# Performance work log

Measured on AMD Instinct MI355X. Metric: run time of the kernel, lower is better.

Reference implementation:

```python
import jax, jax.numpy as jnp
import numpy as np

B, N, DIM, H, D = 1, 1024, 512, 8, 64
BC, BS, K, W = 16, 16, 8, 256   # compress blk, selection blk, top-k blocks, sliding window
C = N // BC                     # number of compression / selection blocks
SCALE = D ** -0.5
EPS = 1e-6
NEG = -1e30


def rmsnorm(x):
    return x * jax.lax.rsqrt(jnp.mean(x * x, axis=-1, keepdims=True) + EPS)


def rope(x):  # x: [B,H,N,D], GPT-NeoX style half rotation
    half = D // 2
    inv = 1.0 / (10000.0 ** (jnp.arange(half, dtype=jnp.float32) / half))
    ang = jnp.arange(x.shape[2], dtype=jnp.float32)[:, None] * inv
    cos, sin = jnp.cos(ang), jnp.sin(ang)
    x1, x2 = x[..., :half], x[..., half:]
    return jnp.concatenate([x1 * cos - x2 * sin, x2 * cos + x1 * sin], axis=-1).astype(x.dtype)


def setup_inputs():
    key = jax.random.key(0)
    ks = jax.random.split(key, 24)
    w = lambda k, shape, fan: jax.random.normal(k, shape, jnp.float32) * (fan ** -0.5)
    return {
        'x':  jax.random.normal(ks[0], (B, N, DIM), jnp.float32),
        've': jax.random.normal(ks[1], (B, N, DIM), jnp.float32),
        'x0': jax.random.normal(ks[2], (B, N, DIM), jnp.float32),
        'lambdas': jnp.array([1.0, 0.0], jnp.float32),
        'Wq': w(ks[3], (DIM, H * D), DIM),
        'Wk': w(ks[4], (DIM, H * D), DIM),
        'Wv': w(ks[5], (DIM, H * D), DIM),
        'Wo': w(ks[6], (H * D, DIM), H * D),
        'Wg': w(ks[7], (DIM, 3 * H), DIM),
        'k_pos': w(ks[8], (H, BC, D), D),
        'v_pos': w(ks[9], (H, BC, D), D),
        'Wck': w(ks[10], (BC * D, D), BC * D),
        'bck': jnp.zeros((D,), jnp.float32),
        'Wcv': w(ks[11], (BC * D, D), BC * D),
        'bcv': jnp.zeros((D,), jnp.float32),
        'k_mem': w(ks[12], (H, 1, D), D),
        'v_mem': w(ks[13], (H, 1, D), D),
        'W1': w(ks[14], (DIM, 4 * DIM), DIM),
        'W2': w(ks[15], (4 * DIM, DIM), 4 * DIM),
    }


def _nsa_attn(xn, Wq, Wk, Wv, Wo, Wg, k_pos, v_pos, Wck, bck, Wcv, bcv, k_mem, v_mem):
    q = (xn @ Wq).reshape(B, N, H, D).transpose(0, 2, 1, 3)   # [B,H,N,D]
    k = (xn @ Wk).reshape(B, N, H, D).transpose(0, 2, 1, 3)
    v = (xn @ Wv).reshape(B, N, H, D).transpose(0, 2, 1, 3)
    q, k = rope(q), rope(k)
    i_idx = jnp.arange(N)

    # ---- compressed branch: pool kv into blocks via learned linear + intra-block pos emb ----
    kb = k.reshape(B, H, C, BC, D) + k_pos[None, :, None]
    vb = v.reshape(B, H, C, BC, D) + v_pos[None, :, None]
    ck = kb.reshape(B, H, C, BC * D) @ Wck + bck              # [B,H,C,D]
    cv = vb.reshape(B, H, C, BC * D) @ Wcv + bcv
    ckf = jnp.concatenate([jnp.broadcast_to(k_mem[None], (B, H, 1, D)), ck], axis=2)
    cvf = jnp.concatenate([jnp.broadcast_to(v_mem[None], (B, H, 1, D)), cv], axis=2)
    csim = jnp.einsum('bhid,bhjd->bhij', q, ckf) * SCALE      # [B,H,N,C+1]
    past = ((jnp.arange(C) + 1) * BC - 1)[None, :] < i_idx[:, None]   # block fully in the past
    cmask = jnp.concatenate([jnp.ones((N, 1), bool), past], axis=1)   # mem kv always visible
    cattn = jax.nn.softmax(jnp.where(cmask[None, None], csim, NEG), axis=-1)
    c_out = jnp.einsum('bhij,bhjd->bhid', cattn, cvf)

    # ---- fine selection branch: top-K blocks by compressed attention importance ----
    imp = jnp.where(past[None, None], cattn[..., 1:], NEG)    # [B,H,N,C]
    vals, sel = jax.lax.top_k(imp, K)                         # [B,H,N,K]
    valid = vals >= 0.0                                       # drop picks among masked blocks
    kb_f = k.reshape(B, H, C, BS, D)
    vb_f = v.reshape(B, H, C, BS, D)
    k_sel = jnp.take_along_axis(kb_f[:, :, None], sel[..., None, None], axis=3)  # [B,H,N,K,BS,D]
    v_sel = jnp.take_along_axis(vb_f[:, :, None], sel[..., None, None], axis=3)
    own = i_idx // BS                                         # query's own block, causal inside
    k_fine = jnp.concatenate([k_sel, kb_f[:, :, own][:, :, :, None]], axis=3)    # [B,H,N,K+1,BS,D]
    v_fine = jnp.concatenate([v_sel, vb_f[:, :, own][:, :, :, None]], axis=3)
    offs = jnp.arange(BS)
    m_sel = (sel[..., None] * BS + offs <= i_idx[None, None, :, None, None]) & valid[..., None]
    m_own = jnp.broadcast_to((own[:, None] * BS + offs <= i_idx[:, None])[None, None, :, None], (B, H, N, 1, BS))
    m_fine = jnp.concatenate([m_sel, m_own], axis=3)
    fsim = jnp.where(m_fine, jnp.einsum('bhnd,bhnksd->bhnks', q, k_fine) * SCALE, NEG)
    fattn = jax.nn.softmax(fsim.reshape(B, H, N, (K + 1) * BS), axis=-1).reshape(B, H, N, K + 1, BS)
    f_out = jnp.einsum('bhnks,bhnksd->bhnd', fattn, v_fine)

    # ---- sliding window branch ----
    smask = (i_idx[None, :] <= i_idx[:, None]) & (i_idx[:, None] - i_idx[None, :] < W)
    ssim = jnp.where(smask[None, None], jnp.einsum('bhid,bhjd->bhij', q, k) * SCALE, NEG)
    s_out = jnp.einsum('bhij,bhjd->bhid', jax.nn.softmax(ssim, axis=-1), v)

    # ---- per-head sigmoid gates combine the three strategies ----
    gates = jax.nn.sigmoid(xn @ Wg).reshape(B, N, H, 3).transpose(0, 2, 1, 3)  # [B,H,N,3]
    o = gates[..., 0:1] * c_out + gates[..., 1:2] * f_out + gates[..., 2:3] * s_out
    return o.transpose(0, 2, 1, 3).reshape(B, N, H * D) @ Wo


def reference(x, ve, x0, lambdas, Wq, Wk, Wv, Wo, Wg, k_pos, v_pos, Wck, bck, Wcv, bcv, k_mem, v_mem, W1, W2):
    # ve is accepted by NSABlock.forward but never consumed in this block
    x = lambdas[0] * x + lambdas[1] * x0
    x = x + _nsa_attn(rmsnorm(x), Wq, Wk, Wv, Wo, Wg, k_pos, v_pos, Wck, bck, Wcv, bcv, k_mem, v_mem)
    x = x + jnp.square(jax.nn.relu(rmsnorm(x) @ W1)) @ W2
    return x
```

## Files before the change

kernel.cpp:

```cpp
#include <hip/hip_runtime.h>
#include <math.h>

#define NTOK 1024
#define DIMM 512
#define NH 8
#define HD 64
#define BCB 16
#define BSB 16
#define KSEL 8
#define WWIN 256
#define CBLK 64
#define SCALE 0.125f
#define EPSV 1e-6f
#define NEGV -1e30f

typedef short bf16x8 __attribute__((ext_vector_type(8)));
typedef float f32x4 __attribute__((ext_vector_type(4)));

__device__ inline ushort f2b(float f) {
  union { float f; unsigned int u; } c; c.f = f;
  unsigned int u = c.u;
  return (ushort)((u + 0x7FFFu + ((u >> 16) & 1u)) >> 16);
}
__device__ inline float b2f(ushort h) {
  union { unsigned int u; float f; } c; c.u = ((unsigned int)h) << 16;
  return c.f;
}

__device__ inline float wred_max(float v) {
#pragma unroll
  for (int off = 1; off < 64; off <<= 1) v = fmaxf(v, __shfl_xor(v, off));
  return v;
}
__device__ inline float wred_sum(float v) {
#pragma unroll
  for (int off = 1; off < 64; off <<= 1) v += __shfl_xor(v, off);
  return v;
}

struct WtrDesc { const float* src; ushort* dh; ushort* dl; int K; int Nsrc; int Npad; };
struct WtrPack { WtrDesc d[9]; int cum[9]; };

__global__ void __launch_bounds__(256)
k_pre(WtrPack pk, const float* __restrict__ x, const float* __restrict__ x0,
      const float* __restrict__ lam, float* __restrict__ xr,
      ushort* __restrict__ xnh, ushort* __restrict__ xnl,
      float* __restrict__ ctab, float* __restrict__ stab,
      const float* __restrict__ k_pos, const float* __restrict__ v_pos,
      const float* __restrict__ Wck, const float* __restrict__ Wcv,
      const float* __restrict__ bck, const float* __restrict__ bcv,
      float* __restrict__ pwk, float* __restrict__ pwv) {
  __shared__ float t[32][33];
  __shared__ float sm[8];
  __shared__ float red[4][64];
  int bid = blockIdx.x, tid = threadIdx.x;
  if (bid < pk.cum[8]) {
    int gb = bid;
    int e = 0;
    while (gb >= pk.cum[e]) e++;
    int start = e ? pk.cum[e - 1] : 0;
    WtrDesc dd = pk.d[e];
    int local = gb - start;
    int XT = dd.Npad >> 5;
    int bx = local % XT, by = local / XT;
    int n0 = bx * 32, k0 = by * 32;
    int tx = tid & 31, ty = tid >> 5;
#pragma unroll
    for (int i = 0; i < 32; i += 8)
      t[ty + i][tx] = (n0 + tx < dd.Nsrc)
          ? dd.src[(size_t)(k0 + ty + i) * dd.Nsrc + n0 + tx] : 0.f;
    __syncthreads();
#pragma unroll
    for (int i = 0; i < 32; i += 8) {
      float vv = t[tx][ty + i];
      ushort h = f2b(vv);
      size_t di = (size_t)(n0 + ty + i) * dd.K + k0 + tx;
      dd.dh[di] = h;
      if (dd.dl) dd.dl[di] = f2b(vv - b2f(h));
    }
  } else if (bid < pk.cum[8] + NTOK) {
    int row = bid - pk.cum[8];
    float l0 = lam[0], l1 = lam[1];
    size_t b = (size_t)row * DIMM;
    float a0 = l0 * x[b + tid]       + l1 * x0[b + tid];
    float a1 = l0 * x[b + tid + 256] + l1 * x0[b + tid + 256];
    xr[b + tid] = a0; xr[b + tid + 256] = a1;
    float ss = a0 * a0 + a1 * a1;
    for (int o = 32; o > 0; o >>= 1) ss += __shfl_down(ss, o);
    int lane = tid & 63, wid = tid >> 6;
    if (lane == 0) sm[wid] = ss;
    __syncthreads();
    if (tid == 0) {
      float s = sm[0] + sm[1] + sm[2] + sm[3];
      sm[0] = rsqrtf(s / (float)DIMM + EPSV);
    }
    __syncthreads();
    float r = sm[0];
    float v0 = a0 * r, v1 = a1 * r;
    ushort h0 = f2b(v0), h1 = f2b(v1);
    xnh[b + tid] = h0;        xnh[b + tid + 256] = h1;
    xnl[b + tid] = f2b(v0 - b2f(h0));
    xnl[b + tid + 256] = f2b(v1 - b2f(h1));
  } else if (bid < pk.cum[8] + NTOK + 128) {
    int g = (bid - pk.cum[8] - NTOK) * 256 + tid;
    int n = g >> 5, d = g & 31;
    float inv = powf(10000.f, -(float)d / 32.f);
    float sn, cs;
    sincosf((float)n * inv, &sn, &cs);
    ctab[g] = cs; stab[g] = sn;
  } else {
    int idx2 = bid - pk.cum[8] - NTOK - 128;
    int h = idx2 & 7, kv = idx2 >> 3;
    const float* pos = kv ? v_pos : k_pos;
    const float* W = kv ? Wcv : Wck;
    const float* bias = kv ? bcv : bck;
    float* pw = kv ? pwv : pwk;
    int d = tid & 63, part = tid >> 6;
    float s = 0.f;
    for (int i = 0; i < 256; i++) {
      int kk = part * 256 + i;
      s += pos[h * 1024 + kk] * W[(size_t)kk * 64 + d];
    }
    red[part][d] = s;
    __syncthreads();
    if (part == 0)
      pw[h * 64 + d] = red[0][d] + red[1][d] + red[2][d] + red[3][d] + bias[d];
  }
}

__global__ void __launch_bounds__(256)
k_rms_bf(const float* __restrict__ xr, const float* __restrict__ p0,
         const float* __restrict__ p1, float* __restrict__ outb,
         ushort* __restrict__ y) {
  int row = blockIdx.x, tid = threadIdx.x;
  size_t b = (size_t)row * DIMM;
  float a0 = xr[b + tid]       + p0[b + tid]       + p1[b + tid];
  float a1 = xr[b + tid + 256] + p0[b + tid + 256] + p1[b + tid + 256];
  outb[b + tid] = a0; outb[b + tid + 256] = a1;
  float ss = a0 * a0 + a1 * a1;
  __shared__ float sm[8];
  for (int o = 32; o > 0; o >>= 1) ss += __shfl_down(ss, o);
  int lane = tid & 63, wid = tid >> 6;
  if (lane == 0) sm[wid] = ss;
  __syncthreads();
  if (tid == 0) {
    float s = sm[0] + sm[1] + sm[2] + sm[3];
    sm[0] = rsqrtf(s / (float)DIMM + EPSV);
  }
  __syncthreads();
  float r = sm[0];
  y[b + tid] = f2b(a0 * r); y[b + tid + 256] = f2b(a1 * r);
}

__global__ void __launch_bounds__(256)
k_gemm_w1(const ushort* __restrict__ A, const ushort* __restrict__ BT,
          ushort* __restrict__ Co) {
  const int Kd = 512, Nd = 2048;
  __shared__ ushort As[128 * 40];
  __shared__ ushort Bs[64 * 40];
  int tid = threadIdx.x;
  int lane = tid & 63, w = tid >> 6;
  int rb = blockIdx.y * 128, cb = blockIdx.x * 64;
  int wm = (w >> 1) * 64, wn = (w & 1) * 32;
  int quad = lane >> 4, l15 = lane & 15;
  int srA = tid >> 1, scA = (tid & 1) * 16;
  int srB = tid >> 2, scB = (tid & 3) * 8;

  f32x4 acc[4][2];
#pragma unroll
  for (int i = 0; i < 4; i++)
#pragma unroll
    for (int j = 0; j < 2; j++) acc[i][j] = (f32x4){0.f, 0.f, 0.f, 0.f};

  const ushort* ap = A  + (size_t)(rb + srA) * Kd + scA;
  const ushort* bp = BT + (size_t)(cb + srB) * Kd + scB;
  ushort* aw = &As[srA * 40 + scA];
  ushort* bw = &Bs[srB * 40 + scB];

  int4 pa0 = *(const int4*)ap;
  int4 pa1 = *(const int4*)(ap + 8);
  int4 pb  = *(const int4*)bp;

  for (int k0 = 0; k0 < Kd; k0 += 32) {
    if (k0) __syncthreads();
    *(int4*)aw = pa0; *(int4*)(aw + 8) = pa1;
    *(int4*)bw = pb;
    __syncthreads();
    if (k0 + 32 < Kd) {
      pa0 = *(const int4*)(ap + k0 + 32);
      pa1 = *(const int4*)(ap + k0 + 40);
      pb  = *(const int4*)(bp + k0 + 32);
    }
    bf16x8 af[4], bfr[2];
#pragma unroll
    for (int t = 0; t < 4; t++)
      af[t] = *(const bf16x8*)&As[(wm + t * 16 + l15) * 40 + quad * 8];
#pragma unroll
    for (int t = 0; t < 2; t++)
      bfr[t] = *(const bf16x8*)&Bs[(wn + t * 16 + l15) * 40 + quad * 8];
#pragma unroll
    for (int i = 0; i < 4; i++)
#pragma unroll
      for (int j = 0; j < 2; j++)
        acc[i][j] = __builtin_amdgcn_mfma_f32_16x16x32_bf16(af[i], bfr[j],
                                                            acc[i][j], 0, 0, 0);
  }

#pragma unroll
  for (int i = 0; i < 4; i++) {
#pragma unroll
    for (int j = 0; j < 2; j++) {
      int col = cb + wn + j * 16 + l15;
#pragma unroll
      for (int r = 0; r < 4; r++) {
        int row = rb + wm + i * 16 + quad * 4 + r;
        float t = fmaxf(acc[i][j][r], 0.f);
        Co[(size_t)row * Nd + col] = f2b(t * t);
      }
    }
  }
}

__global__ void __launch_bounds__(256)
k_gemm_w2(const ushort* __restrict__ A, const ushort* __restrict__ BT,
          float* __restrict__ outb) {
  const int Kd = 2048;
  __shared__ ushort As[64 * 40];
  __shared__ ushort Bs[64 * 40];
  int tid = threadIdx.x;
  int lane = tid & 63, w = tid >> 6;
  int rb = blockIdx.y * 64, cb = blockIdx.x * 64;
  int kb = blockIdx.z * 1024;
  int wm = (w >> 1) * 32, wn = (w & 1) * 32;
  int quad = lane >> 4, l15 = lane & 15;
  int srow = tid >> 2, scol = (tid & 3) * 8;

  f32x4 acc[2][2];
#pragma unroll
  for (int i = 0; i < 2; i++)
#pragma unroll
    for (int j = 0; j < 2; j++) acc[i][j] = (f32x4){0.f, 0.f, 0.f, 0.f};

  const ushort* ap = A  + (size_t)(rb + srow) * Kd + kb + scol;
  const ushort* bp = BT + (size_t)(cb + srow) * Kd + kb + scol;
  ushort* aw = &As[srow * 40 + scol];
  ushort* bw = &Bs[srow * 40 + scol];

  int4 pa = *(const int4*)ap;
  int4 pb = *(const int4*)bp;

  for (int k0 = 0; k0 < 1024; k0 += 32) {
    if (k0) __syncthreads();
    *(int4*)aw = pa;
    *(int4*)bw = pb;
    __syncthreads();
    if (k0 + 32 < 1024) {
      pa = *(const int4*)(ap + k0 + 32);
      pb = *(const int4*)(bp + k0 + 32);
    }
    bf16x8 af[2], bfr[2];
#pragma unroll
    for (int t = 0; t < 2; t++) {
      af[t]  = *(const bf16x8*)&As[(wm + t * 16 + l15) * 40 + quad * 8];
      bfr[t] = *(const bf16x8*)&Bs[(wn + t * 16 + l15) * 40 + quad * 8];
    }
#pragma unroll
    for (int i = 0; i < 2; i++)
#pragma unroll
      for (int j = 0; j < 2; j++)
        acc[i][j] = __builtin_amdgcn_mfma_f32_16x16x32_bf16(af[i], bfr[j],
                                                            acc[i][j], 0, 0, 0);
  }

#pragma unroll
  for (int i = 0; i < 2; i++) {
#pragma unroll
    for (int j = 0; j < 2; j++) {
      int col = cb + wn + j * 16 + l15;
#pragma unroll
      for (int r = 0; r < 4; r++) {
        int row = rb + wm + i * 16 + quad * 4 + r;
        atomicAdd(&outb[(size_t)row * 512 + col], acc[i][j][r]);
      }
    }
  }
}

__global__ void __launch_bounds__(256)
k_gemm_wo(const float* __restrict__ cg, const float* __restrict__ fg,
          const float* __restrict__ sg, const float* __restrict__ gates,
          const ushort* __restrict__ BT, float* __restrict__ P0,
          float* __restrict__ P1) {
  __shared__ ushort As[64 * 40];
  __shared__ ushort Bs[64 * 40];
  int tid = threadIdx.x;
  int lane = tid & 63, wave = tid >> 6;
  int rb = blockIdx.y * 64, cb = blockIdx.x * 64;
  int kb = blockIdx.z * 256;
  int wm = (wave >> 1) * 32, wn = (wave & 1) * 32;
  int q = lane >> 4, l15 = lane & 15;
  int srow = tid >> 2, scol = (tid & 3) * 8;

  f32x4 acc[2][2];
#pragma unroll
  for (int i = 0; i < 2; i++)
#pragma unroll
    for (int j = 0; j < 2; j++) acc[i][j] = (f32x4){0.f, 0.f, 0.f, 0.f};

  int row = rb + srow;
  const ushort* bp = BT + (size_t)(cb + srow) * 512 + kb + scol;
  ushort* aw = &As[srow * 40 + scol];
  ushort* bw = &Bs[srow * 40 + scol];

  for (int k0 = 0; k0 < 256; k0 += 32) {
    int colb = kb + k0 + scol;
    int hh = colb >> 6;
    const float* gp = gates + (size_t)row * 24 + hh * 3;
    float g0 = gp[0], g1 = gp[1], g2 = gp[2];
    size_t off = (size_t)row * 512 + colb;
    float4 c0 = *(const float4*)(cg + off), c1 = *(const float4*)(cg + off + 4);
    float4 f0 = *(const float4*)(fg + off), f1 = *(const float4*)(fg + off + 4);
    float4 s0 = *(const float4*)(sg + off), s1 = *(const float4*)(sg + off + 4);
    float va[8] = {g0 * c0.x + g1 * f0.x + g2 * s0.x,
                   g0 * c0.y + g1 * f0.y + g2 * s0.y,
                   g0 * c0.z + g1 * f0.z + g2 * s0.z,
                   g0 * c0.w + g1 * f0.w + g2 * s0.w,
                   g0 * c1.x + g1 * f1.x + g2 * s1.x,
                   g0 * c1.y + g1 * f1.y + g2 * s1.y,
                   g0 * c1.z + g1 * f1.z + g2 * s1.z,
                   g0 * c1.w + g1 * f1.w + g2 * s1.w};
    ushort h[8];
#pragma unroll
    for (int e = 0; e < 8; e++) h[e] = f2b(va[e]);
    *(int4*)aw = *(int4*)h;
    *(int4*)bw = *(const int4*)(bp + k0);
    __syncthreads();
    bf16x8 af[2], bfr[2];
#pragma unroll
    for (int t = 0; t < 2; t++) {
      af[t]  = *(const bf16x8*)&As[(wm + t * 16 + l15) * 40 + q * 8];
      bfr[t] = *(const bf16x8*)&Bs[(wn + t * 16 + l15) * 40 + q * 8];
    }
#pragma unroll
    for (int i = 0; i < 2; i++)
#pragma unroll
      for (int j = 0; j < 2; j++)
        acc[i][j] = __builtin_amdgcn_mfma_f32_16x16x32_bf16(af[i], bfr[j],
                                                            acc[i][j], 0, 0, 0);
    __syncthreads();
  }

  float* pbuf = blockIdx.z ? P1 : P0;
#pragma unroll
  for (int i = 0; i < 2; i++) {
#pragma unroll
    for (int j = 0; j < 2; j++) {
      int col = cb + wn + j * 16 + l15;
#pragma unroll
      for (int r = 0; r < 4; r++) {
        int rr = rb + wm + i * 16 + q * 4 + r;
        pbuf[(size_t)rr * 512 + col] = acc[i][j][r];
      }
    }
  }
}

__global__ void __launch_bounds__(256)
k_gemm_qkv(const ushort* __restrict__ Ah, const ushort* __restrict__ Al,
           const ushort* __restrict__ BTh, const ushort* __restrict__ BTl,
           float* __restrict__ qout, ushort* __restrict__ khm_h,
           ushort* __restrict__ khm_l, ushort* __restrict__ vhm_h,
           ushort* __restrict__ vhm_l, float* __restrict__ gates,
           const float* __restrict__ ctab, const float* __restrict__ stab) {
  const int Kd = 512;
  __shared__ ushort SM[15360];
  ushort* Ash = SM;
  ushort* Asl = SM + 5120;
  ushort* Bsh = SM + 10240;
  ushort* Bsl = SM + 12800;
  int tid = threadIdx.x;
  int lane = tid & 63, wave = tid >> 6;
  int rb = blockIdx.y * 128, cb = blockIdx.x * 64;
  const bool prec = (cb < 1024);
  int wm = (wave >> 1) * 64, wn = (wave & 1) * 32;
  int q = lane >> 4, l15 = lane & 15;
  int srA = tid >> 1, scA = (tid & 1) * 16;
  int srB = tid >> 2, scB = (tid & 3) * 8;

  f32x4 acc[4][2];
#pragma unroll
  for (int i = 0; i < 4; i++)
#pragma unroll
    for (int j = 0; j < 2; j++) acc[i][j] = (f32x4){0.f, 0.f, 0.f, 0.f};

  const ushort* aph = Ah  + (size_t)(rb + srA) * Kd + scA;
  const ushort* apl = Al  + (size_t)(rb + srA) * Kd + scA;
  const ushort* bph = BTh + (size_t)(cb + srB) * Kd + scB;
  const ushort* bpl = BTl + (size_t)(cb + srB) * Kd + scB;
  ushort* awh = &Ash[srA * 40 + scA];
  ushort* awl = &Asl[srA * 40 + scA];
  ushort* bwh = &Bsh[srB * 40 + scB];
  ushort* bwl = &Bsl[srB * 40 + scB];

  int4 ph0 = *(const int4*)aph;
  int4 ph1 = *(const int4*)(aph + 8);
  int4 pbh = *(const int4*)bph;
  int4 pl0, pl1, pbl;
  if (prec) {
    pl0 = *(const int4*)apl;
    pl1 = *(const int4*)(apl + 8);
    pbl = *(const int4*)bpl;
  }

  for (int k0 = 0; k0 < Kd; k0 += 32) {
    if (k0) __syncthreads();
    *(int4*)awh = ph0; *(int4*)(awh + 8) = ph1;
    *(int4*)bwh = pbh;
    if (prec) {
      *(int4*)awl = pl0; *(int4*)(awl + 8) = pl1;
      *(int4*)bwl = pbl;
    }
    __syncthreads();
    if (k0 + 32 < Kd) {
      ph0 = *(const int4*)(aph + k0 + 32);
      ph1 = *(const int4*)(aph + k0 + 40);
      pbh = *(const int4*)(bph + k0 + 32);
      if (prec) {
        pl0 = *(const int4*)(apl + k0 + 32);
        pl1 = *(const int4*)(apl + k0 + 40);
        pbl = *(const int4*)(bpl + k0 + 32);
      }
    }
    bf16x8 afh[4], bfh[2], afl[4], bfl[2];
#pragma unroll
    for (int t = 0; t < 4; t++)
      afh[t] = *(const bf16x8*)&Ash[(wm + t * 16 + l15) * 40 + q * 8];
#pragma unroll
    for (int t = 0; t < 2; t++)
      bfh[t] = *(const bf16x8*)&Bsh[(wn + t * 16 + l15) * 40 + q * 8];
    if (prec) {
#pragma unroll
      for (int t = 0; t < 4; t++)
        afl[t] = *(const bf16x8*)&Asl[(wm + t * 16 + l15) * 40 + q * 8];
#pragma unroll
      for (int t = 0; t < 2; t++)
        bfl[t] = *(const bf16x8*)&Bsl[(wn + t * 16 + l15) * 40 + q * 8];
    }
#pragma unroll
    for (int i = 0; i < 4; i++)
#pragma unroll
      for (int j = 0; j < 2; j++) {
        acc[i][j] = __builtin_amdgcn_mfma_f32_16x16x32_bf16(afh[i], bfh[j],
                                                            acc[i][j], 0, 0, 0);
        if (prec) {
          acc[i][j] = __builtin_amdgcn_mfma_f32_16x16x32_bf16(afh[i], bfl[j],
                                                              acc[i][j], 0, 0, 0);
          acc[i][j] = __builtin_amdgcn_mfma_f32_16x16x32_bf16(afl[i], bfh[j],
                                                              acc[i][j], 0, 0, 0);
        }
      }
  }

  if (prec) {
    float* st = (float*)SM;
    int h = (cb & 511) >> 6;
#pragma unroll
    for (int hb = 0; hb < 2; hb++) {
      __syncthreads();
      if ((wave >> 1) == hb) {
#pragma unroll
        for (int i = 0; i < 4; i++)
#pragma unroll
          for (int j = 0; j < 2; j++)
#pragma unroll
            for (int r = 0; r < 4; r++)
              st[(i * 16 + q * 4 + r) * 66 + wn + j * 16 + l15] = acc[i][j][r];
      }
      __syncthreads();
#pragma unroll
      for (int e = 0; e < 8; e++) {
        int p = e * 256 + tid;
        int rw = p >> 5, d = p & 31;
        int n = rb + hb * 64 + rw;
        float x1 = st[rw * 66 + d], x2 = st[rw * 66 + d + 32];
        float cs = ctab[n * 32 + d], sn = stab[n * 32 + d];
        float o1 = x1 * cs - x2 * sn;
        float o2 = x2 * cs + x1 * sn;
        if (cb < 512) {
          qout[(size_t)n * 512 + h * 64 + d]      = o1;
          qout[(size_t)n * 512 + h * 64 + d + 32] = o2;
        } else {
          size_t ob = (size_t)h * 65536 + (size_t)n * 64 + d;
          ushort b1 = f2b(o1), b2v = f2b(o2);
          khm_h[ob]      = b1;
          khm_h[ob + 32] = b2v;
          khm_l[ob]      = f2b(o1 - b2f(b1));
          khm_l[ob + 32] = f2b(o2 - b2f(b2v));
        }
      }
    }
  } else {
#pragma unroll
    for (int i = 0; i < 4; i++) {
#pragma unroll
      for (int j = 0; j < 2; j++) {
        int col = cb + wn + j * 16 + l15;
#pragma unroll
        for (int r = 0; r < 4; r++) {
          int row = rb + wm + i * 16 + q * 4 + r;
          float vv = acc[i][j][r];
          if (cb >= 1536) {
            int c24 = col - 1536;
            if (c24 < 24)
              gates[(size_t)row * 24 + c24] = 1.f / (1.f + expf(-vv));
          } else {
            int c = col - 1024;
            size_t ob = (size_t)(c >> 6) * 65536 + (size_t)row * 64 + (c & 63);
            ushort hb = f2b(vv);
            vhm_h[ob] = hb;
            vhm_l[ob] = f2b(vv - b2f(hb));
          }
        }
      }
    }
  }
}

__global__ void __launch_bounds__(256)
k_mid(const ushort* __restrict__ khm_h, const ushort* __restrict__ khm_l,
      const ushort* __restrict__ vhm_h, const ushort* __restrict__ vhm_l,
      const ushort* __restrict__ WckTh, const ushort* __restrict__ WckTl,
      const ushort* __restrict__ WcvTh, const ushort* __restrict__ WcvTl,
      const float* __restrict__ pwk, const float* __restrict__ pwv,
      float* __restrict__ ckb, float* __restrict__ cvb,
      const float* __restrict__ qg, float* __restrict__ sout) {
  __shared__ union {
    struct { ushort Ash[32 * 72]; ushort Asl[32 * 72];
             ushort Bsh[64 * 72]; ushort Bsl[64 * 72]; } c;
    struct { ushort Kt[64 * 72]; ushort VT[64 * 72];
             ushort Qs[64 * 72]; ushort Ps[4][16 * 72]; } s;
  } U;
  int tid = threadIdx.x, lane = tid & 63, w = tid >> 6;
  int quad = lane >> 4, l15 = lane & 15;

  if (blockIdx.x < 32) {
    int h = blockIdx.x & 7, kv = (blockIdx.x >> 3) & 1, mh = blockIdx.x >> 4;
    const ushort* sH = kv ? vhm_h : khm_h;
    const ushort* sL = kv ? vhm_l : khm_l;
    const ushort* WTh = kv ? WcvTh : WckTh;
    const ushort* WTl = kv ? WcvTl : WckTl;
    const float* pw = (kv ? pwv : pwk) + h * 64;
    float* outp = kv ? cvb : ckb;

    ushort* Ash = U.c.Ash; ushort* Asl = U.c.Asl;
    ushort* Bsh = U.c.Bsh; ushort* Bsl = U.c.Bsl;
    int wmi = w >> 1, wnj = w & 1;
    int arow = tid >> 3, ae0 = (tid & 7) * 8;
    int brow = tid >> 2, be0 = (tid & 3) * 16;
    size_t abase = (size_t)h * 65536 + (size_t)(mh * 32 + arow) * 1024 + ae0;
    size_t bbase = (size_t)brow * 1024 + be0;

    f32x4 acc[2];
#pragma unroll
    for (int j = 0; j < 2; j++) acc[j] = (f32x4){0.f, 0.f, 0.f, 0.f};

    for (int t = 0; t < 16; t++) {
      int kb = t * 64;
      *(int4*)&Ash[arow * 72 + ae0] = *(const int4*)(sH + abase + kb);
      *(int4*)&Asl[arow * 72 + ae0] = *(const int4*)(sL + abase + kb);
      *(int4*)&Bsh[brow * 72 + be0]     = *(const int4*)(WTh + bbase + kb);
      *(int4*)&Bsh[brow * 72 + be0 + 8] = *(const int4*)(WTh + bbase + kb + 8);
      *(int4*)&Bsl[brow * 72 + be0]     = *(const int4*)(WTl + bbase + kb);
      *(int4*)&Bsl[brow * 72 + be0 + 8] = *(const int4*)(WTl + bbase + kb + 8);
      __syncthreads();
#pragma unroll
      for (int sub = 0; sub < 2; sub++) {
        int ar2 = (wmi * 16 + l15) * 72 + sub * 32 + quad * 8;
        bf16x8 afh = *(const bf16x8*)&Ash[ar2];
        bf16x8 afl = *(const bf16x8*)&Asl[ar2];
#pragma unroll
        for (int j = 0; j < 2; j++) {
          int br2 = (wnj * 32 + j * 16 + l15) * 72 + sub * 32 + quad * 8;
          bf16x8 bfh = *(const bf16x8*)&Bsh[br2];
          bf16x8 bfl = *(const bf16x8*)&Bsl[br2];
          acc[j] = __builtin_amdgcn_mfma_f32_16x16x32_bf16(afh, bfh, acc[j], 0, 0, 0);
          acc[j] = __builtin_amdgcn_mfma_f32_16x16x32_bf16(afh, bfl, acc[j], 0, 0, 0);
          acc[j] = __builtin_amdgcn_mfma_f32_16x16x32_bf16(afl, bfh, acc[j], 0, 0, 0);
        }
      }
      __syncthreads();
    }

#pragma unroll
    for (int j = 0; j < 2; j++) {
      int d = wnj * 32 + j * 16 + l15;
      float bv = pw[d];
#pragma unroll
      for (int r = 0; r < 4; r++) {
        int c = mh * 32 + wmi * 16 + quad * 4 + r;
        outp[((size_t)h * 64 + c) * 64 + d] = acc[j][r] + bv;
      }
    }
  } else {
    int sidx = blockIdx.x - 32;
    int h = sidx >> 4, i0 = (sidx & 15) * 64;
    ushort* Kt = U.s.Kt; ushort* VT = U.s.VT; ushort* Qs = U.s.Qs;

#pragma unroll
    for (int it = 0; it < 2; it++) {
      int f = it * 256 + tid;
      int r = f >> 3, d0 = (f & 7) * 8;
      const float* qp = qg + (size_t)(i0 + r) * DIMM + h * HD + d0;
      float4 t0 = *(const float4*)qp;
      float4 t1 = *(const float4*)(qp + 4);
      ushort u[8] = {f2b(t0.x), f2b(t0.y), f2b(t0.z), f2b(t0.w),
                     f2b(t1.x), f2b(t1.y), f2b(t1.z), f2b(t1.w)};
      *(int4*)&Qs[r * 72 + d0] = *(int4*)u;
    }

    int lo = i0 - (WWIN - 1); if (lo < 0) lo = 0;
    int jb_lo = lo >> 6, jb_hi = (i0 + 63) >> 6;

    float mrow[4], lrow[4];
    f32x4 Of[4];
#pragma unroll
    for (int r = 0; r < 4; r++) { mrow[r] = NEGV; lrow[r] = 0.f; }
#pragma unroll
    for (int d = 0; d < 4; d++) Of[d] = (f32x4){0.f, 0.f, 0.f, 0.f};

    for (int jb = jb_lo; jb <= jb_hi; jb++) {
      __syncthreads();
#pragma unroll
      for (int it = 0; it < 2; it++) {
        int f = it * 256 + tid;
        int r = f >> 3, c8 = (f & 7) * 8;
        const ushort* kp = khm_h + (size_t)h * 65536 + (size_t)(jb * 64 + r) * 64 + c8;
        *(int4*)&Kt[r * 72 + c8] = *(const int4*)kp;
        const ushort* vp = vhm_h + (size_t)h * 65536 + (size_t)(jb * 64 + r) * 64 + c8;
        ushort vv[8];
        *(int4*)vv = *(const int4*)vp;
#pragma unroll
        for (int e = 0; e < 8; e++) VT[(c8 + e) * 72 + r] = vv[e];
      }
      __syncthreads();

      bf16x8 qa[2];
#pragma unroll
      for (int c = 0; c < 2; c++)
        qa[c] = *(const bf16x8*)&Qs[(w * 16 + l15) * 72 + c * 32 + quad * 8];

      f32x4 sc[4];
      __builtin_amdgcn_s_setprio(1);
#pragma unroll
      for (int ks = 0; ks < 4; ks++) {
        f32x4 a = (f32x4){0.f, 0.f, 0.f, 0.f};
#pragma unroll
        for (int c = 0; c < 2; c++) {
          bf16x8 kb = *(const bf16x8*)&Kt[(ks * 16 + l15) * 72 + c * 32 + quad * 8];
          a = __builtin_amdgcn_mfma_f32_16x16x32_bf16(qa[c], kb, a, 0, 0, 0);
        }
        sc[ks] = a;
      }
      __builtin_amdgcn_s_setprio(0);

      float pm[4][4], rmax[4];
#pragma unroll
      for (int r = 0; r < 4; r++) rmax[r] = NEGV;
#pragma unroll
      for (int ks = 0; ks < 4; ks++) {
        int gj = jb * 64 + ks * 16 + l15;
#pragma unroll
        for (int r = 0; r < 4; r++) {
          int qi = i0 + w * 16 + quad * 4 + r;
          bool vis = (gj <= qi) && (qi - gj < WWIN);
          float s = vis ? sc[ks][r] * SCALE : NEGV;
          pm[ks][r] = s;
          rmax[r] = fmaxf(rmax[r], s);
        }
      }
#pragma unroll
      for (int off = 1; off < 16; off <<= 1)
#pragma unroll
        for (int r = 0; r < 4; r++)
          rmax[r] = fmaxf(rmax[r], __shfl_xor(rmax[r], off));

      float alpha[4], rsum[4];
#pragma unroll
      for (int r = 0; r < 4; r++) {
        float newm = fmaxf(mrow[r], rmax[r]);
        alpha[r] = expf(mrow[r] - newm);
        mrow[r] = newm;
        rsum[r] = 0.f;
      }
#pragma unroll
      for (int ks = 0; ks < 4; ks++)
#pragma unroll
        for (int r = 0; r < 4; r++) {
          float p = expf(pm[ks][r] - mrow[r]);
          pm[ks][r] = p;
          rsum[r] += p;
        }
#pragma unroll
      for (int off = 1; off < 16; off <<= 1)
#pragma unroll
        for (int r = 0; r < 4; r++)
          rsum[r] += __shfl_xor(rsum[r], off);
#pragma unroll
      for (int r = 0; r < 4; r++)
        lrow[r] = lrow[r] * alpha[r] + rsum[r];

#pragma unroll
      for (int ks = 0; ks < 4; ks++)
#pragma unroll
        for (int r = 0; r < 4; r++)
          U.s.Ps[w][(quad * 4 + r) * 72 + ks * 16 + l15] = f2b(pm[ks][r]);
#pragma unroll
      for (int d = 0; d < 4; d++)
#pragma unroll
        for (int r = 0; r < 4; r++)
          Of[d][r] *= alpha[r];

      __builtin_amdgcn_s_setprio(1);
#pragma unroll
      for (int c = 0; c < 2; c++) {
        bf16x8 pa = *(const bf16x8*)&U.s.Ps[w][l15 * 72 + c * 32 + quad * 8];
#pragma unroll
        for (int d = 0; d < 4; d++) {
          bf16x8 vb = *(const bf16x8*)&VT[(d * 16 + l15) * 72 + c * 32 + quad * 8];
          Of[d] = __builtin_amdgcn_mfma_f32_16x16x32_bf16(pa, vb, Of[d], 0, 0, 0);
        }
      }
      __builtin_amdgcn_s_setprio(0);
    }

#pragma unroll
    for (int d = 0; d < 4; d++)
#pragma unroll
      for (int r = 0; r < 4; r++) {
        int qi = i0 + w * 16 + quad * 4 + r;
        sout[(size_t)qi * DIMM + h * HD + d * 16 + l15] = Of[d][r] / lrow[r];
      }
  }
}

__global__ void __launch_bounds__(256)
k_cmp(const float* __restrict__ qg, const float* __restrict__ ckb,
      const float* __restrict__ cvb, const float* __restrict__ k_mem,
      const float* __restrict__ v_mem, float* __restrict__ cout,
      int* __restrict__ sel) {
  int h = blockIdx.y, i0 = blockIdx.x * 16;
  int tid = threadIdx.x, lane = tid & 63, w = tid >> 6;
  __shared__ float ckt[64][65];
  __shared__ float cvs[64][65];
  __shared__ float qs[16][64];
  __shared__ float kms[64], vms[64];
  __shared__ float sp[4][64];

#pragma unroll
  for (int r = 0; r < 4; r++) {
    int f = r * 256 + tid;
    int c = f >> 4, d0 = (f & 15) * 4;
    float4 t = *(const float4*)(ckb + ((size_t)h * 64 + c) * 64 + d0);
    ckt[d0][c] = t.x; ckt[d0 + 1][c] = t.y; ckt[d0 + 2][c] = t.z; ckt[d0 + 3][c] = t.w;
    float4 u = *(const float4*)(cvb + ((size_t)h * 64 + c) * 64 + d0);
    cvs[c][d0] = u.x; cvs[c][d0 + 1] = u.y; cvs[c][d0 + 2] = u.z; cvs[c][d0 + 3] = u.w;
  }
  {
    int r = tid >> 4, d0 = (tid & 15) * 4;
    float4 t = *(const float4*)(qg + (size_t)(i0 + r) * DIMM + h * HD + d0);
    qs[r][d0] = t.x; qs[r][d0 + 1] = t.y; qs[r][d0 + 2] = t.z; qs[r][d0 + 3] = t.w;
  }
  if (tid < 64) kms[tid] = k_mem[h * HD + tid];
  else if (tid < 128) vms[tid - 64] = v_mem[h * HD + tid - 64];
  __syncthreads();

  for (int s = 0; s < 4; s++) {
    int ql = w * 4 + s, qi = i0 + ql;
    float dot = 0.f, dm = 0.f;
#pragma unroll 8
    for (int e = 0; e < 64; e++) {
      float qe = qs[ql][e];
      dot = fmaf(qe, ckt[e][lane], dot);
      dm  = fmaf(qe, kms[e], dm);
    }
    bool vis = (lane * BCB + BCB - 1) < qi;
    float sj = vis ? dot * SCALE : NEGV;
    float smem = dm * SCALE;
    float m = wred_max(fmaxf(sj, smem));
    float p = expf(sj - m);
    float pmem = expf(smem - m);
    float l = wred_sum(p) + pmem;
    float inv = 1.f / l;

    float impv = vis ? p : NEGV;
#pragma unroll
    for (int kk = 0; kk < KSEL; kk++) {
      float bv = impv; int bi = lane;
#pragma unroll
      for (int off = 32; off > 0; off >>= 1) {
        float ov = __shfl_xor(bv, off);
        int   oi = __shfl_xor(bi, off);
        if (ov > bv || (ov == bv && oi < bi)) { bv = ov; bi = oi; }
      }
      if (lane == 0) sel[((size_t)h * NTOK + qi) * KSEL + kk] = (bv >= 0.f) ? bi : -1;
      if (lane == bi) impv = NEGV;
    }

    sp[w][lane] = p;
    float od = pmem * vms[lane];
#pragma unroll 8
    for (int j = 0; j < 64; j++) od = fmaf(sp[w][j], cvs[j][lane], od);
    cout[(size_t)qi * DIMM + h * HD + lane] = od * inv;
  }
}

__global__ void __launch_bounds__(256)
k_fine(const float* __restrict__ qg, const ushort* __restrict__ khm_bf,
       const ushort* __restrict__ vhm_bf, const int* __restrict__ sel,
       float* __restrict__ fout) {
  int i = blockIdx.x, h = blockIdx.y;
  int tid = threadIdx.x, lane = tid & 63, w = tid >> 6;
  __shared__ float qsh[64];
  __shared__ ushort vsb[144 * 64];
  __shared__ float sp[144];
  __shared__ int selS[8];
  __shared__ float mred[4], sredS[4];
  __shared__ float pacc[4][64];

  int own = i >> 4;
  if (tid < 64) qsh[tid] = qg[(size_t)i * DIMM + h * HD + tid];
  if (tid >= 64 && tid < 72)
    selS[tid - 64] = sel[((size_t)h * NTOK + i) * KSEL + tid - 64];
  __syncthreads();

  const ushort* kbase = khm_bf + (size_t)h * 65536;
  const ushort* vbase = vhm_bf + (size_t)h * 65536;

#pragma unroll
  for (int it = 0; it < 5; it++) {
    int idx = it * 256 + tid;
    if (idx < 1152) {
      int row = idx >> 3, c8 = (idx & 7) * 8;
      int kk = row >> 4;
      int bidx = (kk < KSEL) ? selS[kk] : own;
      if (bidx < 0) bidx = 0;
      *(int4*)&vsb[row * 64 + c8] =
          *(const int4*)(vbase + (size_t)(bidx * BSB + (row & 15)) * 64 + c8);
    }
  }

  float s_loc = NEGV;
  bool active = (tid < 144);
  if (active) {
    int kk = tid >> 4;
    int bidx; bool vis;
    if (kk < KSEL) {
      bidx = selS[kk];
      vis = (bidx >= 0);
      if (!vis) bidx = 0;
    } else {
      bidx = own;
      vis = (tid - 128) <= (i & 15);
    }
    const ushort* kr = kbase + (size_t)(bidx * BSB + (tid & 15)) * 64;
    float dot = 0.f;
#pragma unroll
    for (int e8 = 0; e8 < 8; e8++) {
      ushort kv[8];
      *(int4*)kv = *(const int4*)(kr + e8 * 8);
#pragma unroll
      for (int e = 0; e < 8; e++)
        dot = fmaf(qsh[e8 * 8 + e], b2f(kv[e]), dot);
    }
    s_loc = vis ? dot * SCALE : NEGV;
  }
  float mw = wred_max(s_loc);
  if (lane == 0) mred[w] = mw;
  __syncthreads();
  float m = fmaxf(fmaxf(mred[0], mred[1]), fmaxf(mred[2], mred[3]));
  float p = active ? expf(s_loc - m) : 0.f;
  float sw = wred_sum(p);
  if (lane == 0) sredS[w] = sw;
  if (active) sp[tid] = p;
  __syncthreads();
  float l = sredS[0] + sredS[1] + sredS[2] + sredS[3];

  float acc = 0.f;
  int j0 = w * 36;
#pragma unroll 6
  for (int jj = 0; jj < 36; jj++) {
    int j = j0 + jj;
    acc = fmaf(sp[j], b2f(vsb[j * 64 + lane]), acc);
  }
  pacc[w][lane] = acc;
  __syncthreads();
  if (w == 0)
    fout[(size_t)i * DIMM + h * HD + lane] =
        (pacc[0][lane] + pacc[1][lane] + pacc[2][lane] + pacc[3][lane]) / l;
}

extern "C" void kernel_launch(void* const* d_in, const int* in_sizes, int n_in,
                              void* d_out, int out_size, void* d_ws, size_t ws_size,
                              hipStream_t stream) {
  const float* x     = (const float*)d_in[0];
  const float* ve    = (const float*)d_in[1]; (void)ve;
  const float* x0    = (const float*)d_in[2];
  const float* lam   = (const float*)d_in[3];
  const float* Wq    = (const float*)d_in[4];
  const float* Wk    = (const float*)d_in[5];
  const float* Wv    = (const float*)d_in[6];
  const float* Wo    = (const float*)d_in[7];
  const float* Wg    = (const float*)d_in[8];
  const float* k_pos = (const float*)d_in[9];
  const float* v_pos = (const float*)d_in[10];
  const float* Wck   = (const float*)d_in[11];
  const float* bck   = (const float*)d_in[12];
  const float* Wcv   = (const float*)d_in[13];
  const float* bcv   = (const float*)d_in[14];
  const float* k_mem = (const float*)d_in[15];
  const float* v_mem = (const float*)d_in[16];
  const float* W1    = (const float*)d_in[17];
  const float* W2    = (const float*)d_in[18];
  float* out = (float*)d_out;
  float* ws  = (float*)d_ws;

  const size_t NW = (size_t)NTOK * DIMM;
  float* xr    = ws;
  float* xn    = ws + 1 * NW;
  float* q     = ws + 2 * NW;
  float* kslot = ws + 3 * NW;
  float* vslot = ws + 4 * NW;
  float* coutb = ws + 5 * NW;
  float* foutb = ws + 6 * NW;
  float* soutb = ws + 7 * NW;
  float* gates = ws + 9 * NW;
  float* ckb   = gates + 32768;
  float* cvb   = ckb + 32768;
  int*   selb  = (int*)(cvb + 32768);
  ushort* qkvTh = (ushort*)(cvb + 32768 + 65536);
  ushort* qkvTl = qkvTh + 1600 * 512;
  ushort* WoT   = qkvTl + 1600 * 512;
  ushort* W1T   = WoT   + 512 * 512;
  ushort* W2T   = W1T   + 2048 * 512;
  ushort* WckTh = W2T   + 512 * 2048;
  ushort* WckTl = WckTh + 64 * 1024;
  ushort* WcvTh = WckTl + 64 * 1024;
  ushort* WcvTl = WcvTh + 64 * 1024;
  float* ctab   = (float*)(WcvTl + 64 * 1024);
  float* stab   = ctab + 32768;
  float* pwk    = stab + 32768;
  float* pwv    = pwk + 512;

  ushort* xnh = (ushort*)xn;
  ushort* xnl = xnh + NW;
  ushort* khm_h = (ushort*)kslot;
  ushort* khm_l = khm_h + 524288;
  ushort* vhm_h = (ushort*)vslot;
  ushort* vhm_l = vhm_h + 524288;
  float* p0w = kslot;
  float* p1w = q;
  ushort* ybf = (ushort*)soutb;
  ushort* h1b = (ushort*)q;

  WtrPack pk;
  pk.d[0] = {Wq, qkvTh,              qkvTl,              512, 512,  512};
  pk.d[1] = {Wk, qkvTh + 512 * 512,  qkvTl + 512 * 512,  512, 512,  512};
  pk.d[2] = {Wv, qkvTh + 1024 * 512, qkvTl + 1024 * 512, 512, 512,  512};
  pk.d[3] = {Wo, WoT, nullptr,  512, 512,  512};
  pk.d[4] = {W1, W1T, nullptr,  512, 2048, 2048};
  pk.d[5] = {W2, W2T, nullptr, 2048, 512,  512};
  pk.d[6] = {Wck, WckTh, WckTl, 1024, 64, 64};
  pk.d[7] = {Wcv, WcvTh, WcvTl, 1024, 64, 64};
  pk.d[8] = {Wg, qkvTh + 1536 * 512, qkvTl + 1536 * 512, 512, 24, 64};
  int cum = 0;
  for (int e = 0; e < 9; e++) {
    cum += (pk.d[e].Npad / 32) * (pk.d[e].K / 32);
    pk.cum[e] = cum;
  }

  k_pre<<<cum + NTOK + 128 + 16, 256, 0, stream>>>(
      pk, x, x0, lam, xr, xnh, xnl, ctab, stab,
      k_pos, v_pos, Wck, Wcv, bck, bcv, pwk, pwv);

  k_gemm_qkv<<<dim3(25, NTOK / 128), 256, 0, stream>>>(
      xnh, xnl, qkvTh, qkvTl, q, khm_h, khm_l, vhm_h, vhm_l, gates,
      ctab, stab);

  k_mid<<<160, 256, 0, stream>>>(khm_h, khm_l, vhm_h, vhm_l,
                                 WckTh, WckTl, WcvTh, WcvTl,
                                 pwk, pwv, ckb, cvb, q, soutb);

  k_cmp<<<dim3(NTOK / 16, NH), 256, 0, stream>>>(q, ckb, cvb, k_mem, v_mem,
                                                 coutb, selb);

  k_fine<<<dim3(NTOK, NH), 256, 0, stream>>>(q, khm_h, vhm_h, selb, foutb);

  k_gemm_wo<<<dim3(512 / 64, NTOK / 64, 2), 256, 0, stream>>>(
      coutb, foutb, soutb, gates, WoT, p0w, p1w);
  k_rms_bf<<<NTOK, 256, 0, stream>>>(xr, p0w, p1w, out, ybf);

  k_gemm_w1<<<dim3(2048 / 64, NTOK / 128), 256, 0, stream>>>(ybf, W1T, h1b);
  k_gemm_w2<<<dim3(512 / 64, NTOK / 64, 2), 256, 0, stream>>>(h1b, W2T, out);
}
```

Baseline: 251.2 us.

## Fuse fine-selection attention into compressed-attention kernel, keep top-k in registers

```diff
diff --git a/kernel.cpp b/kernel.cpp
--- a/kernel.cpp
+++ b/kernel.cpp
@@ -744,10 +744,11 @@
 }
 
 __global__ void __launch_bounds__(256)
-k_cmp(const float* __restrict__ qg, const float* __restrict__ ckb,
-      const float* __restrict__ cvb, const float* __restrict__ k_mem,
-      const float* __restrict__ v_mem, float* __restrict__ cout,
-      int* __restrict__ sel) {
+k_cmpf(const float* __restrict__ qg, const float* __restrict__ ckb,
+       const float* __restrict__ cvb, const float* __restrict__ k_mem,
+       const float* __restrict__ v_mem, const ushort* __restrict__ khm_h,
+       const ushort* __restrict__ vhm_h, float* __restrict__ cout,
+       float* __restrict__ fout) {
   int h = blockIdx.y, i0 = blockIdx.x * 16;
   int tid = threadIdx.x, lane = tid & 63, w = tid >> 6;
   __shared__ float ckt[64][65];
@@ -755,6 +756,7 @@
   __shared__ float qs[16][64];
   __shared__ float kms[64], vms[64];
   __shared__ float sp[4][64];
+  __shared__ float spf[4][144];
 
 #pragma unroll
   for (int r = 0; r < 4; r++) {
@@ -773,6 +775,9 @@
   if (tid < 64) kms[tid] = k_mem[h * HD + tid];
   else if (tid < 128) vms[tid - 64] = v_mem[h * HD + tid - 64];
   __syncthreads();
+
+  const ushort* kbase = khm_h + (size_t)h * 65536;
+  const ushort* vbase = vhm_h + (size_t)h * 65536;
 
   for (int s = 0; s < 4; s++) {
     int ql = w * 4 + s, qi = i0 + ql;
@@ -792,6 +797,7 @@
     float l = wred_sum(p) + pmem;
     float inv = 1.f / l;
 
+    int selreg = -1;
     float impv = vis ? p : NEGV;
 #pragma unroll
     for (int kk = 0; kk < KSEL; kk++) {
@@ -802,7 +808,7 @@
         int   oi = __shfl_xor(bi, off);
         if (ov > bv || (ov == bv && oi < bi)) { bv = ov; bi = oi; }
       }
-      if (lane == 0) sel[((size_t)h * NTOK + qi) * KSEL + kk] = (bv >= 0.f) ? bi : -1;
+      if (lane == kk) selreg = (bv >= 0.f) ? bi : -1;
       if (lane == bi) impv = NEGV;
     }
 
@@ -811,92 +817,64 @@
 #pragma unroll 8
     for (int j = 0; j < 64; j++) od = fmaf(sp[w][j], cvs[j][lane], od);
     cout[(size_t)qi * DIMM + h * HD + lane] = od * inv;
-  }
-}
-
-__global__ void __launch_bounds__(256)
-k_fine(const float* __restrict__ qg, const ushort* __restrict__ khm_bf,
-       const ushort* __restrict__ vhm_bf, const int* __restrict__ sel,
-       float* __restrict__ fout) {
-  int i = blockIdx.x, h = blockIdx.y;
-  int tid = threadIdx.x, lane = tid & 63, w = tid >> 6;
-  __shared__ float qsh[64];
-  __shared__ ushort vsb[144 * 64];
-  __shared__ float sp[144];
-  __shared__ int selS[8];
-  __shared__ float mred[4], sredS[4];
-  __shared__ float pacc[4][64];
-
-  int own = i >> 4;
-  if (tid < 64) qsh[tid] = qg[(size_t)i * DIMM + h * HD + tid];
-  if (tid >= 64 && tid < 72)
-    selS[tid - 64] = sel[((size_t)h * NTOK + i) * KSEL + tid - 64];
-  __syncthreads();
-
-  const ushort* kbase = khm_bf + (size_t)h * 65536;
-  const ushort* vbase = vhm_bf + (size_t)h * 65536;
-
-#pragma unroll
-  for (int it = 0; it < 5; it++) {
-    int idx = it * 256 + tid;
-    if (idx < 1152) {
-      int row = idx >> 3, c8 = (idx & 7) * 8;
-      int kk = row >> 4;
-      int bidx = (kk < KSEL) ? selS[kk] : own;
+
+    int own = qi >> 4;
+    float slv[3];
+#pragma unroll
+    for (int t = 0; t < 3; t++) {
+      int key = t * 64 + lane;
+      float sv = NEGV;
+      if (key < 144) {
+        int kk = key >> 4, krow = key & 15;
+        int bidx; bool fvis;
+        if (kk < KSEL) {
+          bidx = __shfl(selreg, kk);
+          fvis = (bidx >= 0);
+          if (!fvis) bidx = 0;
+        } else {
+          bidx = own;
+          fvis = (krow <= (qi & 15));
+        }
+        const ushort* kr = kbase + (size_t)(bidx * BSB + krow) * 64;
+        float fd = 0.f;
+#pragma unroll
+        for (int e8 = 0; e8 < 8; e8++) {
+          ushort kv8[8];
+          *(int4*)kv8 = *(const int4*)(kr + e8 * 8);
+#pragma unroll
+          for (int e = 0; e < 8; e++)
+            fd = fmaf(qs[ql][e8 * 8 + e], b2f(kv8[e]), fd);
+        }
+        sv = fvis ? fd * SCALE : NEGV;
+      }
+      slv[t] = sv;
+    }
+    float fm = wred_max(fmaxf(fmaxf(slv[0], slv[1]), slv[2]));
+    float fsum = 0.f;
+#pragma unroll
+    for (int t = 0; t < 3; t++) {
+      int key = t * 64 + lane;
+      if (key < 144) {
+        float pv = expf(slv[t] - fm);
+        spf[w][key] = pv;
+        fsum += pv;
+      }
+    }
+    fsum = wred_sum(fsum);
+    float finv = 1.f / fsum;
+
+    float facc = 0.f;
+#pragma unroll
+    for (int kk = 0; kk < KSEL + 1; kk++) {
+      int bidx = (kk < KSEL) ? __shfl(selreg, kk) : own;
       if (bidx < 0) bidx = 0;
-      *(int4*)&vsb[row * 64 + c8] =
-          *(const int4*)(vbase + (size_t)(bidx * BSB + (row & 15)) * 64 + c8);
-    }
-  }
-
-  float s_loc = NEGV;
-  bool active = (tid < 144);
-  if (active) {
-    int kk = tid >> 4;
-    int bidx; bool vis;
-    if (kk < KSEL) {
-      bidx = selS[kk];
-      vis = (bidx >= 0);
-      if (!vis) bidx = 0;
-    } else {
-      bidx = own;
-      vis = (tid - 128) <= (i & 15);
-    }
-    const ushort* kr = kbase + (size_t)(bidx * BSB + (tid & 15)) * 64;
-    float dot = 0.f;
-#pragma unroll
-    for (int e8 = 0; e8 < 8; e8++) {
-      ushort kv[8];
-      *(int4*)kv = *(const int4*)(kr + e8 * 8);
-#pragma unroll
-      for (int e = 0; e < 8; e++)
-        dot = fmaf(qsh[e8 * 8 + e], b2f(kv[e]), dot);
-    }
-    s_loc = vis ? dot * SCALE : NEGV;
-  }
-  float mw = wred_max(s_loc);
-  if (lane == 0) mred[w] = mw;
-  __syncthreads();
-  float m = fmaxf(fmaxf(mred[0], mred[1]), fmaxf(mred[2], mred[3]));
-  float p = active ? expf(s_loc - m) : 0.f;
-  float sw = wred_sum(p);
-  if (lane == 0) sredS[w] = sw;
-  if (active) sp[tid] = p;
-  __syncthreads();
-  float l = sredS[0] + sredS[1] + sredS[2] + sredS[3];
-
-  float acc = 0.f;
-  int j0 = w * 36;
-#pragma unroll 6
-  for (int jj = 0; jj < 36; jj++) {
-    int j = j0 + jj;
-    acc = fmaf(sp[j], b2f(vsb[j * 64 + lane]), acc);
-  }
-  pacc[w][lane] = acc;
-  __syncthreads();
-  if (w == 0)
-    fout[(size_t)i * DIMM + h * HD + lane] =
-        (pacc[0][lane] + pacc[1][lane] + pacc[2][lane] + pacc[3][lane]) / l;
+      const ushort* vr = vbase + (size_t)(bidx * BSB) * 64 + lane;
+#pragma unroll 4
+      for (int krow = 0; krow < 16; krow++)
+        facc = fmaf(spf[w][kk * 16 + krow], b2f(vr[(size_t)krow * 64]), facc);
+    }
+    fout[(size_t)qi * DIMM + h * HD + lane] = facc * finv;
+  }
 }
 
 extern "C" void kernel_launch(void* const* d_in, const int* in_sizes, int n_in,
@@ -936,7 +914,6 @@
   float* gates = ws + 9 * NW;
   float* ckb   = gates + 32768;
   float* cvb   = ckb + 32768;
-  int*   selb  = (int*)(cvb + 32768);
   ushort* qkvTh = (ushort*)(cvb + 32768 + 65536);
   ushort* qkvTl = qkvTh + 1600 * 512;
   ushort* WoT   = qkvTl + 1600 * 512;
@@ -990,10 +967,8 @@
                                  WckTh, WckTl, WcvTh, WcvTl,
                                  pwk, pwv, ckb, cvb, q, soutb);
 
-  k_cmp<<<dim3(NTOK / 16, NH), 256, 0, stream>>>(q, ckb, cvb, k_mem, v_mem,
-                                                 coutb, selb);
-
-  k_fine<<<dim3(NTOK, NH), 256, 0, stream>>>(q, khm_h, vhm_h, selb, foutb);
+  k_cmpf<<<dim3(NTOK / 16, NH), 256, 0, stream>>>(
+      q, ckb, cvb, k_mem, v_mem, khm_h, vhm_h, coutb, foutb);
 
   k_gemm_wo<<<dim3(512 / 64, NTOK / 64, 2), 256, 0, stream>>>(
       coutb, foutb, soutb, gates, WoT, p0w, p1w);
```

Result: no change. 252.8 us (+0.6%).
